# Performance work log

Measured on AMD Instinct MI355X. Metric: run time of the kernel, lower is better.

Reference implementation:

```python
import jax, jax.numpy as jnp
import numpy as np

B, T, C, H = 4, 4096, 2048, 128  # batch, seq, emb_dim, head_size


def setup_inputs() -> dict:
    key = jax.random.key(0)
    k1, k2, k3, k4 = jax.random.split(key, 4)
    idx = jax.random.normal(k1, (B, T, C), dtype=jnp.float32)
    # nn.Linear weight layout: [out_features, in_features]; scale like torch init
    s = 1.0 / np.sqrt(C)
    Wq = jax.random.uniform(k2, (H, C), jnp.float32, -s, s)
    Wk = jax.random.uniform(k3, (H, C), jnp.float32, -s, s)
    Wv = jax.random.uniform(k4, (H, C), jnp.float32, -s, s)
    return {"idx": idx, "Wq": Wq, "Wk": Wk, "Wv": Wv}


def reference(idx, Wq, Wk, Wv):
    b, t, c = idx.shape
    q = jnp.einsum('btc,hc->bth', idx, Wq)  # [B,T,H]
    k = jnp.einsum('btc,hc->bth', idx, Wk)
    v = jnp.einsum('btc,hc->bth', idx, Wv)
    # NOTE: original computes keys @ queries^T and scales by emb_dim**-0.5
    scale = jnp.asarray(c, idx.dtype) ** -0.5
    wei = jnp.einsum('bih,bjh->bij', k, q) * scale  # [B,T,T]
    causal = jnp.tril(jnp.ones((t, t), dtype=bool))
    wei = jnp.where(causal, wei, -jnp.inf)
    wei = jax.nn.softmax(wei, axis=-1)
    return jnp.einsum('bij,bjh->bih', wei, v)  # [B,T,H]
```

## Files before the change

### kernel.cpp

```cpp
#include <hip/hip_runtime.h>
#include <hip/hip_bf16.h>
#include <cstdint>

#define TSEQ 4096
#define CDIM 2048
#define HDIM 128

typedef short bf8v __attribute__((ext_vector_type(8)));
typedef float f4v  __attribute__((ext_vector_type(4)));

__device__ __forceinline__ unsigned short f2b(float f) {
  union { float f; unsigned u; } v; v.f = f;
  unsigned u = v.u;
  return (unsigned short)((u + 0x7fffu + ((u >> 16) & 1u)) >> 16);
}

__device__ __forceinline__ f4v mfma16(bf8v a, bf8v b, f4v c) {
  return __builtin_amdgcn_mfma_f32_16x16x32_bf16(a, b, c, 0, 0, 0);
}

__global__ void wcat_kernel(const float* __restrict__ Wq, const float* __restrict__ Wk,
                            const float* __restrict__ Wv, unsigned short* __restrict__ Wcat) {
  int e = (blockIdx.x * 256 + threadIdx.x) * 4;
  int n = e >> 11;
  int k = e & 2047;
  const float* src;
  if (n < 128)      src = Wq + (size_t)n * CDIM + k;
  else if (n < 256) src = Wk + (size_t)(n - 128) * CDIM + k;
  else              src = Wv + (size_t)(n - 256) * CDIM + k;
  float4 f = *(const float4*)src;
  ushort4 o;
  o.x = f2b(f.x); o.y = f2b(f.y); o.z = f2b(f.z); o.w = f2b(f.w);
  *(ushort4*)(Wcat + e) = o;
}

__global__ __launch_bounds__(512, 6) void proj_gemm(const float* __restrict__ A,
                                                    const unsigned short* __restrict__ Bw,
                                                    unsigned short* __restrict__ QB,
                                                    unsigned short* __restrict__ KA,
                                                    unsigned short* __restrict__ VB) {
  __shared__ union {
    struct { unsigned short As[2][64][40]; unsigned short Bs[2][128][40]; } st;
    unsigned short Ct[64][132];
  } sm;
  const int m0 = blockIdx.x * 64;
  const int y  = blockIdx.y;
  const int n0 = y * 128;
  const int tid = threadIdx.x;
  const int lane = tid & 63;
  const int w = tid >> 6;
  const int wm = (w & 1) * 32, wn = (w >> 1) * 32;
  const int llo = lane & 15, lhi = lane >> 4;

  f4v acc[2][2];
#pragma unroll
  for (int i = 0; i < 2; ++i)
#pragma unroll
    for (int j = 0; j < 2; ++j) acc[i][j] = (f4v){0.f, 0.f, 0.f, 0.f};

  const int arow = tid >> 3, acol = (tid & 7) * 4;
  const int brow = tid >> 2, bcol = (tid & 3) * 8;
  const float* aptr = A + (size_t)(m0 + arow) * CDIM + acol;
  const unsigned short* bptr = Bw + (size_t)(n0 + brow) * CDIM + bcol;

  float4 fa = *(const float4*)(aptr);
  uint4  ub = *(const uint4*)(bptr);
  {
    ushort4 o;
    o.x = f2b(fa.x); o.y = f2b(fa.y); o.z = f2b(fa.z); o.w = f2b(fa.w);
    *(ushort4*)&sm.st.As[0][arow][acol] = o;
    *(uint4*)&sm.st.Bs[0][brow][bcol]   = ub;
  }

  for (int it = 0; it < 64; ++it) {
    const int cur = it & 1;
    __syncthreads();
    if (it < 63) {
      fa = *(const float4*)(aptr + (it + 1) * 32);
      ub = *(const uint4*)(bptr + (it + 1) * 32);
    }
    bf8v af[2], bfr[2];
    af[0]  = *(const bf8v*)&sm.st.As[cur][wm + llo][lhi * 8];
    af[1]  = *(const bf8v*)&sm.st.As[cur][wm + 16 + llo][lhi * 8];
    bfr[0] = *(const bf8v*)&sm.st.Bs[cur][wn + llo][lhi * 8];
    bfr[1] = *(const bf8v*)&sm.st.Bs[cur][wn + 16 + llo][lhi * 8];
#pragma unroll
    for (int i = 0; i < 2; ++i)
#pragma unroll
      for (int j = 0; j < 2; ++j) acc[i][j] = mfma16(af[i], bfr[j], acc[i][j]);
    if (it < 63) {
      ushort4 o;
      o.x = f2b(fa.x); o.y = f2b(fa.y); o.z = f2b(fa.z); o.w = f2b(fa.w);
      int nxt = cur ^ 1;
      *(ushort4*)&sm.st.As[nxt][arow][acol] = o;
      *(uint4*)&sm.st.Bs[nxt][brow][bcol]   = ub;
    }
  }
  __syncthreads();
#pragma unroll
  for (int i = 0; i < 2; ++i)
#pragma unroll
    for (int j = 0; j < 2; ++j)
#pragma unroll
      for (int r = 0; r < 4; ++r)
        sm.Ct[wm + i * 16 + lhi * 4 + r][wn + j * 16 + llo] = f2b(acc[i][j][r]);
  __syncthreads();
  if (y < 2) {
    unsigned short* dst = (y == 0) ? QB : KA;
    const size_t base16 = (size_t)(m0 >> 4);
#pragma unroll
    for (int p = 0; p < 2; ++p) {
      int g = p * 512 + tid;
      int t16l = g >> 8, kk = (g >> 6) & 3, ln = g & 63;
      int lo = ln & 15, hi = ln >> 4;
      bf8v v = *(const bf8v*)&sm.Ct[t16l * 16 + lo][kk * 32 + hi * 8];
      *(bf8v*)(dst + (((base16 + t16l) * 4 + kk) * 64 + ln) * 8) = v;
    }
  } else {
    const size_t base32 = (size_t)(m0 >> 5);
#pragma unroll
    for (int p = 0; p < 3; ++p) {
      int g = p * 512 + tid;
      if (g < 1152) {
        int jbl = g / 576;
        int ht  = (g % 576) >> 6;
        int ln  = g & 63;
        int lo = ln & 15, hi = ln >> 4;
        bf8v v;
        if (ht == 8) {
#pragma unroll
          for (int e = 0; e < 8; ++e) v[e] = (lo == 0) ? (short)0x3F80 : (short)0;
        } else {
#pragma unroll
          for (int e = 0; e < 8; ++e) v[e] = (short)sm.Ct[jbl * 32 + hi * 8 + e][ht * 16 + lo];
        }
        *(bf8v*)(VB + (((base32 + jbl) * 9 + ht) * 512 + (size_t)ln * 8)) = v;
      }
    }
  }
}

__global__ __launch_bounds__(256, 4) void attn6(const unsigned short* __restrict__ QB,
                                                const unsigned short* __restrict__ KA,
                                                const unsigned short* __restrict__ VB,
                                                float* __restrict__ out) {
  __shared__ union SM {
    unsigned short Ps[4][2][16][68];
    struct { float Om[4][16][68]; float Lm[4][16]; } mg;
  } sm;
  const int x = blockIdx.x;
  const int b = x & 3;
  const int u = x >> 2;
  const int g = u >> 6, r0 = u & 63;
  const int s = (g & 1) ? (g * 64 + 63 - r0) : (g * 64 + r0);
  const int lastjt = s >> 2;
  const int tid = threadIdx.x;
  const int w = tid >> 6, lane = tid & 63;
  const int llo = lane & 15, lhi = lane >> 4;
  const float scale = 0.022097086912079608f;

  bf8v aK[4];
  {
    const unsigned short* kp = KA + (size_t)(b * 256 + s) * 2048;
#pragma unroll
    for (int kk = 0; kk < 4; ++kk) aK[kk] = *(const bf8v*)(kp + (kk * 64 + lane) * 8);
  }

  f4v Oacc[9];
#pragma unroll
  for (int nt = 0; nt < 9; ++nt) Oacc[nt] = (f4v){0.f, 0.f, 0.f, 0.f};

  auto computeS = [&](int jtS, int buf) {
    const unsigned short* qp = QB + (size_t)(b * 256 + jtS * 4) * 2048;
#pragma unroll
    for (int ct = 0; ct < 4; ++ct) {
      f4v acc = (f4v){0.f, 0.f, 0.f, 0.f};
#pragma unroll
      for (int kk = 0; kk < 4; ++kk) {
        bf8v bq = *(const bf8v*)(qp + ((ct * 4 + kk) * 64 + lane) * 8);
        acc = mfma16(aK[kk], bq, acc);
      }
#pragma unroll
      for (int r = 0; r < 4; ++r) {
        float sv = acc[r];
        if (jtS == lastjt) {
          int j = jtS * 64 + ct * 16 + llo;
          int i = s * 16 + lhi * 4 + r;
          if (j > i) sv = -3.0e38f;
        }
        sm.Ps[w][buf][lhi * 4 + r][ct * 16 + llo] = f2b(__expf(sv * scale));
      }
    }
  };

  if (w <= lastjt) computeS(w, 0);
  int buf = 0;
  for (int jt = w; jt <= lastjt; jt += 4) {
    bf8v aP0 = *(const bf8v*)&sm.Ps[w][buf][llo][lhi * 8];
    bf8v aP1 = *(const bf8v*)&sm.Ps[w][buf][llo][32 + lhi * 8];
    if (jt + 4 <= lastjt) computeS(jt + 4, buf ^ 1);
    const unsigned short* vp = VB + (size_t)(b * 128 + jt * 2) * 4608;
#pragma unroll
    for (int nt = 0; nt < 9; ++nt) {
      f4v o = Oacc[nt];
      o = mfma16(aP0, *(const bf8v*)(vp + nt * 512 + (size_t)lane * 8), o);
      o = mfma16(aP1, *(const bf8v*)(vp + 4608 + nt * 512 + (size_t)lane * 8), o);
      Oacc[nt] = o;
    }
    buf ^= 1;
  }

#pragma unroll
  for (int half = 0; half < 2; ++half) {
    __syncthreads();
#pragma unroll
    for (int nt = 0; nt < 4; ++nt)
#pragma unroll
      for (int r = 0; r < 4; ++r)
        sm.mg.Om[w][lhi * 4 + r][nt * 16 + llo] = Oacc[half * 4 + nt][r];
    if (half == 0 && llo == 0) {
#pragma unroll
      for (int r = 0; r < 4; ++r) sm.mg.Lm[w][lhi * 4 + r] = Oacc[8][r];
    }
    __syncthreads();
    {
      int row = tid >> 4, c0 = (tid & 15) * 4;
      float L = sm.mg.Lm[0][row] + sm.mg.Lm[1][row] + sm.mg.Lm[2][row] + sm.mg.Lm[3][row];
      float inv = 1.0f / L;
      float* op = out + (size_t)(b * TSEQ + s * 16 + row) * HDIM + half * 64 + c0;
#pragma unroll
      for (int e = 0; e < 4; ++e) {
        float o = sm.mg.Om[0][row][c0 + e] + sm.mg.Om[1][row][c0 + e] +
                  sm.mg.Om[2][row][c0 + e] + sm.mg.Om[3][row][c0 + e];
        op[e] = o * inv;
      }
    }
  }
}

extern "C" void kernel_launch(void* const* d_in, const int* in_sizes, int n_in,
                              void* d_out, int out_size, void* d_ws, size_t ws_size,
                              hipStream_t stream) {
  const float* idx = (const float*)d_in[0];
  const float* Wq  = (const float*)d_in[1];
  const float* Wk  = (const float*)d_in[2];
  const float* Wv  = (const float*)d_in[3];
  float* out = (float*)d_out;
  char* ws = (char*)d_ws;
  unsigned short* Wcat = (unsigned short*)ws;
  unsigned short* QB   = (unsigned short*)(ws + ((size_t)2  << 20));
  unsigned short* KA   = (unsigned short*)(ws + ((size_t)7  << 20));
  unsigned short* VB   = (unsigned short*)(ws + ((size_t)12 << 20));

  wcat_kernel<<<768, 256, 0, stream>>>(Wq, Wk, Wv, Wcat);
  proj_gemm<<<dim3(256, 3), 512, 0, stream>>>(idx, Wcat, QB, KA, VB);
  attn6<<<1024, 256, 0, stream>>>(QB, KA, VB, out);
}
```

Before: 291.1 us.

## Fuse QKV projection into one 64x384 tile with async LDS weight loads

The projection GEMM now computes all three Q/K/V outputs in a single block covering 64 rows by 384 columns, instead of launching three column blocks per row tile. This means the fp32 activation tile is read and converted to bf16 once rather than three times. Weight tiles are loaded straight from global memory into LDS with global_load_lds, using an XOR swizzle to avoid bank conflicts, and the K step grows to 64. The cost is fewer blocks (256), much larger LDS use, and lower occupancy (launch bounds 2 instead of 6).

```diff
diff --git a/kernel.cpp b/kernel.cpp
--- a/kernel.cpp
+++ b/kernel.cpp
@@ -17,6 +17,12 @@
 
 __device__ __forceinline__ f4v mfma16(bf8v a, bf8v b, f4v c) {
   return __builtin_amdgcn_mfma_f32_16x16x32_bf16(a, b, c, 0, 0, 0);
+}
+
+__device__ __forceinline__ void gload_lds16(const void* g, void* l) {
+  __builtin_amdgcn_global_load_lds(
+      (const __attribute__((address_space(1))) unsigned int*)g,
+      (__attribute__((address_space(3))) unsigned int*)l, 16, 0, 0);
 }
 
 __global__ void wcat_kernel(const float* __restrict__ Wq, const float* __restrict__ Wk,
@@ -34,89 +40,114 @@
   *(ushort4*)(Wcat + e) = o;
 }
 
-__global__ __launch_bounds__(512, 6) void proj_gemm(const float* __restrict__ A,
+__global__ __launch_bounds__(512, 2) void proj_gemm(const float* __restrict__ A,
                                                     const unsigned short* __restrict__ Bw,
                                                     unsigned short* __restrict__ QB,
                                                     unsigned short* __restrict__ KA,
                                                     unsigned short* __restrict__ VB) {
   __shared__ union {
-    struct { unsigned short As[2][64][40]; unsigned short Bs[2][128][40]; } st;
-    unsigned short Ct[64][132];
+    struct { unsigned short As[2][64][72]; unsigned short Bs[2][384][64]; } st;
+    unsigned short Ct[64][392];
   } sm;
   const int m0 = blockIdx.x * 64;
-  const int y  = blockIdx.y;
-  const int n0 = y * 128;
   const int tid = threadIdx.x;
   const int lane = tid & 63;
   const int w = tid >> 6;
-  const int wm = (w & 1) * 32, wn = (w >> 1) * 32;
   const int llo = lane & 15, lhi = lane >> 4;
 
-  f4v acc[2][2];
-#pragma unroll
-  for (int i = 0; i < 2; ++i)
-#pragma unroll
-    for (int j = 0; j < 2; ++j) acc[i][j] = (f4v){0.f, 0.f, 0.f, 0.f};
-
-  const int arow = tid >> 3, acol = (tid & 7) * 4;
-  const int brow = tid >> 2, bcol = (tid & 3) * 8;
-  const float* aptr = A + (size_t)(m0 + arow) * CDIM + acol;
-  const unsigned short* bptr = Bw + (size_t)(n0 + brow) * CDIM + bcol;
-
-  float4 fa = *(const float4*)(aptr);
-  uint4  ub = *(const uint4*)(bptr);
-  {
-    ushort4 o;
-    o.x = f2b(fa.x); o.y = f2b(fa.y); o.z = f2b(fa.z); o.w = f2b(fa.w);
-    *(ushort4*)&sm.st.As[0][arow][acol] = o;
-    *(uint4*)&sm.st.Bs[0][brow][bcol]   = ub;
-  }
-
-  for (int it = 0; it < 64; ++it) {
+  f4v acc[4][3];
+#pragma unroll
+  for (int i = 0; i < 4; ++i)
+#pragma unroll
+    for (int j = 0; j < 3; ++j) acc[i][j] = (f4v){0.f, 0.f, 0.f, 0.f};
+
+  const int ar0 = tid >> 4;
+  const int ac0 = (tid & 15) * 4;
+  const float* aptr0 = A + (size_t)(m0 + ar0) * CDIM + ac0;
+  const float* aptr1 = A + (size_t)(m0 + 32 + ar0) * CDIM + ac0;
+
+  const int brow = lane >> 3;
+  const int bgs  = (lane & 7) ^ brow;
+  const unsigned short* bptr = Bw + (size_t)(w * 48 + brow) * CDIM + bgs * 8;
+
+  float4 fa0 = *(const float4*)(aptr0);
+  float4 fa1 = *(const float4*)(aptr1);
+#pragma unroll
+  for (int j = 0; j < 6; ++j)
+    gload_lds16(bptr + (size_t)j * 8 * CDIM, &sm.st.Bs[0][w * 48 + j * 8][0]);
+  {
+    ushort4 o0, o1;
+    o0.x = f2b(fa0.x); o0.y = f2b(fa0.y); o0.z = f2b(fa0.z); o0.w = f2b(fa0.w);
+    o1.x = f2b(fa1.x); o1.y = f2b(fa1.y); o1.z = f2b(fa1.z); o1.w = f2b(fa1.w);
+    *(ushort4*)&sm.st.As[0][ar0][ac0]      = o0;
+    *(ushort4*)&sm.st.As[0][32 + ar0][ac0] = o1;
+  }
+
+  for (int it = 0; it < 32; ++it) {
     const int cur = it & 1;
     __syncthreads();
-    if (it < 63) {
-      fa = *(const float4*)(aptr + (it + 1) * 32);
-      ub = *(const uint4*)(bptr + (it + 1) * 32);
-    }
-    bf8v af[2], bfr[2];
-    af[0]  = *(const bf8v*)&sm.st.As[cur][wm + llo][lhi * 8];
-    af[1]  = *(const bf8v*)&sm.st.As[cur][wm + 16 + llo][lhi * 8];
-    bfr[0] = *(const bf8v*)&sm.st.Bs[cur][wn + llo][lhi * 8];
-    bfr[1] = *(const bf8v*)&sm.st.Bs[cur][wn + 16 + llo][lhi * 8];
-#pragma unroll
-    for (int i = 0; i < 2; ++i)
-#pragma unroll
-      for (int j = 0; j < 2; ++j) acc[i][j] = mfma16(af[i], bfr[j], acc[i][j]);
-    if (it < 63) {
-      ushort4 o;
-      o.x = f2b(fa.x); o.y = f2b(fa.y); o.z = f2b(fa.z); o.w = f2b(fa.w);
-      int nxt = cur ^ 1;
-      *(ushort4*)&sm.st.As[nxt][arow][acol] = o;
-      *(uint4*)&sm.st.Bs[nxt][brow][bcol]   = ub;
-    }
-  }
+    if (it < 31) {
+      fa0 = *(const float4*)(aptr0 + (it + 1) * 64);
+      fa1 = *(const float4*)(aptr1 + (it + 1) * 64);
+      const int nxt = cur ^ 1;
+#pragma unroll
+      for (int j = 0; j < 6; ++j)
+        gload_lds16(bptr + (size_t)j * 8 * CDIM + (it + 1) * 64,
+                    &sm.st.Bs[nxt][w * 48 + j * 8][0]);
+    }
+#pragma unroll
+    for (int kk = 0; kk < 2; ++kk) {
+      bf8v af[4], bf[3];
+#pragma unroll
+      for (int i = 0; i < 4; ++i)
+        af[i] = *(const bf8v*)&sm.st.As[cur][i * 16 + llo][kk * 32 + lhi * 8];
+#pragma unroll
+      for (int j = 0; j < 3; ++j) {
+        const int n = w * 48 + j * 16 + llo;
+        bf[j] = *(const bf8v*)&sm.st.Bs[cur][n][(((kk << 2) + lhi) ^ (llo & 7)) * 8];
+      }
+#pragma unroll
+      for (int i = 0; i < 4; ++i)
+#pragma unroll
+        for (int j = 0; j < 3; ++j) acc[i][j] = mfma16(af[i], bf[j], acc[i][j]);
+    }
+    if (it < 31) {
+      const int nxt = cur ^ 1;
+      ushort4 o0, o1;
+      o0.x = f2b(fa0.x); o0.y = f2b(fa0.y); o0.z = f2b(fa0.z); o0.w = f2b(fa0.w);
+      o1.x = f2b(fa1.x); o1.y = f2b(fa1.y); o1.z = f2b(fa1.z); o1.w = f2b(fa1.w);
+      *(ushort4*)&sm.st.As[nxt][ar0][ac0]      = o0;
+      *(ushort4*)&sm.st.As[nxt][32 + ar0][ac0] = o1;
+    }
+  }
+
   __syncthreads();
 #pragma unroll
-  for (int i = 0; i < 2; ++i)
-#pragma unroll
-    for (int j = 0; j < 2; ++j)
+  for (int i = 0; i < 4; ++i)
+#pragma unroll
+    for (int j = 0; j < 3; ++j)
 #pragma unroll
       for (int r = 0; r < 4; ++r)
-        sm.Ct[wm + i * 16 + lhi * 4 + r][wn + j * 16 + llo] = f2b(acc[i][j][r]);
+        sm.Ct[i * 16 + lhi * 4 + r][w * 48 + j * 16 + llo] = f2b(acc[i][j][r]);
   __syncthreads();
-  if (y < 2) {
-    unsigned short* dst = (y == 0) ? QB : KA;
+
+  {
     const size_t base16 = (size_t)(m0 >> 4);
 #pragma unroll
-    for (int p = 0; p < 2; ++p) {
-      int g = p * 512 + tid;
-      int t16l = g >> 8, kk = (g >> 6) & 3, ln = g & 63;
-      int lo = ln & 15, hi = ln >> 4;
-      bf8v v = *(const bf8v*)&sm.Ct[t16l * 16 + lo][kk * 32 + hi * 8];
-      *(bf8v*)(dst + (((base16 + t16l) * 4 + kk) * 64 + ln) * 8) = v;
-    }
-  } else {
+    for (int yy = 0; yy < 2; ++yy) {
+      unsigned short* dst = yy ? KA : QB;
+      const int colb = yy * 128;
+#pragma unroll
+      for (int p = 0; p < 2; ++p) {
+        int g = p * 512 + tid;
+        int t16l = g >> 8, kk2 = (g >> 6) & 3, ln = g & 63;
+        int lo = ln & 15, hi = ln >> 4;
+        bf8v v = *(const bf8v*)&sm.Ct[t16l * 16 + lo][colb + kk2 * 32 + hi * 8];
+        *(bf8v*)(dst + (((base16 + t16l) * 4 + kk2) * 64 + ln) * 8) = v;
+      }
+    }
+  }
+  {
     const size_t base32 = (size_t)(m0 >> 5);
 #pragma unroll
     for (int p = 0; p < 3; ++p) {
@@ -132,7 +163,7 @@
           for (int e = 0; e < 8; ++e) v[e] = (lo == 0) ? (short)0x3F80 : (short)0;
         } else {
 #pragma unroll
-          for (int e = 0; e < 8; ++e) v[e] = (short)sm.Ct[jbl * 32 + hi * 8 + e][ht * 16 + lo];
+          for (int e = 0; e < 8; ++e) v[e] = (short)sm.Ct[jbl * 32 + hi * 8 + e][256 + ht * 16 + lo];
         }
         *(bf8v*)(VB + (((base32 + jbl) * 9 + ht) * 512 + (size_t)ln * 8)) = v;
       }
@@ -253,6 +284,6 @@
   unsigned short* VB   = (unsigned short*)(ws + ((size_t)12 << 20));
 
   wcat_kernel<<<768, 256, 0, stream>>>(Wq, Wk, Wv, Wcat);
-  proj_gemm<<<dim3(256, 3), 512, 0, stream>>>(idx, Wcat, QB, KA, VB);
+  proj_gemm<<<256, 512, 0, stream>>>(idx, Wcat, QB, KA, VB);
   attn6<<<1024, 256, 0, stream>>>(QB, KA, VB, out);
 }
```

After: 282.8 us. 2.8% less time.

## Fuse QKV projection into one pass per row tile with MFMA-packed weights

Applied to the files above, without the earlier changes.

The weight-conversion kernel now writes the concatenated bf16 weights pre-swizzled into MFMA fragment order. The projection GEMM drops the 3-way grid split and LDS staging: each 64-row block computes all 384 output columns, and each wave loads its fp32 activation fragments straight from global memory into registers. This reads the large activation tensor once instead of three times and removes per-iteration barriers. In exchange it uses more accumulator registers, has lower occupancy, and does uncoalesced global reads of the B fragments, relying on L2 hits.

```diff
diff --git a/kernel.cpp b/kernel.cpp
--- a/kernel.cpp
+++ b/kernel.cpp
@@ -21,102 +21,106 @@
 
 __global__ void wcat_kernel(const float* __restrict__ Wq, const float* __restrict__ Wk,
                             const float* __restrict__ Wv, unsigned short* __restrict__ Wcat) {
-  int e = (blockIdx.x * 256 + threadIdx.x) * 4;
-  int n = e >> 11;
-  int k = e & 2047;
+  int c = blockIdx.x * 256 + threadIdx.x;
+  int lane = c & 63;
+  int kkg  = (c >> 6) & 63;
+  int nb   = c >> 12;
+  int n  = nb * 16 + (lane & 15);
+  int k0 = kkg * 32 + (lane >> 4) * 8;
   const float* src;
-  if (n < 128)      src = Wq + (size_t)n * CDIM + k;
-  else if (n < 256) src = Wk + (size_t)(n - 128) * CDIM + k;
-  else              src = Wv + (size_t)(n - 256) * CDIM + k;
-  float4 f = *(const float4*)src;
-  ushort4 o;
-  o.x = f2b(f.x); o.y = f2b(f.y); o.z = f2b(f.z); o.w = f2b(f.w);
-  *(ushort4*)(Wcat + e) = o;
-}
-
-__global__ __launch_bounds__(512, 6) void proj_gemm(const float* __restrict__ A,
+  if (n < 128)      src = Wq + (size_t)n * CDIM + k0;
+  else if (n < 256) src = Wk + (size_t)(n - 128) * CDIM + k0;
+  else              src = Wv + (size_t)(n - 256) * CDIM + k0;
+  float4 f0 = ((const float4*)src)[0];
+  float4 f1 = ((const float4*)src)[1];
+  bf8v o;
+  o[0] = (short)f2b(f0.x); o[1] = (short)f2b(f0.y);
+  o[2] = (short)f2b(f0.z); o[3] = (short)f2b(f0.w);
+  o[4] = (short)f2b(f1.x); o[5] = (short)f2b(f1.y);
+  o[6] = (short)f2b(f1.z); o[7] = (short)f2b(f1.w);
+  *(bf8v*)(Wcat + (size_t)c * 8) = o;
+}
+
+__global__ __launch_bounds__(512, 2) void proj_gemm(const float* __restrict__ A,
                                                     const unsigned short* __restrict__ Bw,
                                                     unsigned short* __restrict__ QB,
                                                     unsigned short* __restrict__ KA,
                                                     unsigned short* __restrict__ VB) {
-  __shared__ union {
-    struct { unsigned short As[2][64][40]; unsigned short Bs[2][128][40]; } st;
-    unsigned short Ct[64][132];
-  } sm;
+  __shared__ unsigned short Ct[64][392];
   const int m0 = blockIdx.x * 64;
-  const int y  = blockIdx.y;
-  const int n0 = y * 128;
   const int tid = threadIdx.x;
   const int lane = tid & 63;
   const int w = tid >> 6;
-  const int wm = (w & 1) * 32, wn = (w >> 1) * 32;
+  const int sub = w & 3;
+  const int cg  = w >> 2;
   const int llo = lane & 15, lhi = lane >> 4;
 
-  f4v acc[2][2];
-#pragma unroll
-  for (int i = 0; i < 2; ++i)
-#pragma unroll
-    for (int j = 0; j < 2; ++j) acc[i][j] = (f4v){0.f, 0.f, 0.f, 0.f};
-
-  const int arow = tid >> 3, acol = (tid & 7) * 4;
-  const int brow = tid >> 2, bcol = (tid & 3) * 8;
-  const float* aptr = A + (size_t)(m0 + arow) * CDIM + acol;
-  const unsigned short* bptr = Bw + (size_t)(n0 + brow) * CDIM + bcol;
-
-  float4 fa = *(const float4*)(aptr);
-  uint4  ub = *(const uint4*)(bptr);
+  f4v acc[12];
+#pragma unroll
+  for (int j = 0; j < 12; ++j) acc[j] = (f4v){0.f, 0.f, 0.f, 0.f};
+
+  const float* ap = A + (size_t)(m0 + sub * 16 + llo) * CDIM + lhi * 8;
+
+  float4 fa00 = *(const float4*)(ap);
+  float4 fa01 = *(const float4*)(ap + 4);
+  float4 fa10 = *(const float4*)(ap + 32);
+  float4 fa11 = *(const float4*)(ap + 36);
+
+  const unsigned short* bbase = Bw + (size_t)(cg * 12) * 64 * 64 * 8 + (size_t)lane * 8;
+
+  for (int it = 0; it < 32; ++it) {
+    bf8v af[2];
+    af[0][0] = (short)f2b(fa00.x); af[0][1] = (short)f2b(fa00.y);
+    af[0][2] = (short)f2b(fa00.z); af[0][3] = (short)f2b(fa00.w);
+    af[0][4] = (short)f2b(fa01.x); af[0][5] = (short)f2b(fa01.y);
+    af[0][6] = (short)f2b(fa01.z); af[0][7] = (short)f2b(fa01.w);
+    af[1][0] = (short)f2b(fa10.x); af[1][1] = (short)f2b(fa10.y);
+    af[1][2] = (short)f2b(fa10.z); af[1][3] = (short)f2b(fa10.w);
+    af[1][4] = (short)f2b(fa11.x); af[1][5] = (short)f2b(fa11.y);
+    af[1][6] = (short)f2b(fa11.z); af[1][7] = (short)f2b(fa11.w);
+    if (it < 31) {
+      const float* apn = ap + (it + 1) * 64;
+      fa00 = *(const float4*)(apn);
+      fa01 = *(const float4*)(apn + 4);
+      fa10 = *(const float4*)(apn + 32);
+      fa11 = *(const float4*)(apn + 36);
+    }
+#pragma unroll
+    for (int kk = 0; kk < 2; ++kk) {
+      const int kkg = it * 2 + kk;
+      bf8v bf[12];
+#pragma unroll
+      for (int j = 0; j < 12; ++j)
+        bf[j] = *(const bf8v*)(bbase + ((size_t)j * 64 + kkg) * 64 * 8);
+#pragma unroll
+      for (int j = 0; j < 12; ++j) acc[j] = mfma16(af[kk], bf[j], acc[j]);
+    }
+  }
+
+#pragma unroll
+  for (int j = 0; j < 12; ++j)
+#pragma unroll
+    for (int r = 0; r < 4; ++r)
+      Ct[sub * 16 + lhi * 4 + r][cg * 192 + j * 16 + llo] = f2b(acc[j][r]);
+  __syncthreads();
+
   {
-    ushort4 o;
-    o.x = f2b(fa.x); o.y = f2b(fa.y); o.z = f2b(fa.z); o.w = f2b(fa.w);
-    *(ushort4*)&sm.st.As[0][arow][acol] = o;
-    *(uint4*)&sm.st.Bs[0][brow][bcol]   = ub;
-  }
-
-  for (int it = 0; it < 64; ++it) {
-    const int cur = it & 1;
-    __syncthreads();
-    if (it < 63) {
-      fa = *(const float4*)(aptr + (it + 1) * 32);
-      ub = *(const uint4*)(bptr + (it + 1) * 32);
-    }
-    bf8v af[2], bfr[2];
-    af[0]  = *(const bf8v*)&sm.st.As[cur][wm + llo][lhi * 8];
-    af[1]  = *(const bf8v*)&sm.st.As[cur][wm + 16 + llo][lhi * 8];
-    bfr[0] = *(const bf8v*)&sm.st.Bs[cur][wn + llo][lhi * 8];
-    bfr[1] = *(const bf8v*)&sm.st.Bs[cur][wn + 16 + llo][lhi * 8];
-#pragma unroll
-    for (int i = 0; i < 2; ++i)
-#pragma unroll
-      for (int j = 0; j < 2; ++j) acc[i][j] = mfma16(af[i], bfr[j], acc[i][j]);
-    if (it < 63) {
-      ushort4 o;
-      o.x = f2b(fa.x); o.y = f2b(fa.y); o.z = f2b(fa.z); o.w = f2b(fa.w);
-      int nxt = cur ^ 1;
-      *(ushort4*)&sm.st.As[nxt][arow][acol] = o;
-      *(uint4*)&sm.st.Bs[nxt][brow][bcol]   = ub;
-    }
-  }
-  __syncthreads();
-#pragma unroll
-  for (int i = 0; i < 2; ++i)
-#pragma unroll
-    for (int j = 0; j < 2; ++j)
-#pragma unroll
-      for (int r = 0; r < 4; ++r)
-        sm.Ct[wm + i * 16 + lhi * 4 + r][wn + j * 16 + llo] = f2b(acc[i][j][r]);
-  __syncthreads();
-  if (y < 2) {
-    unsigned short* dst = (y == 0) ? QB : KA;
     const size_t base16 = (size_t)(m0 >> 4);
 #pragma unroll
-    for (int p = 0; p < 2; ++p) {
-      int g = p * 512 + tid;
-      int t16l = g >> 8, kk = (g >> 6) & 3, ln = g & 63;
-      int lo = ln & 15, hi = ln >> 4;
-      bf8v v = *(const bf8v*)&sm.Ct[t16l * 16 + lo][kk * 32 + hi * 8];
-      *(bf8v*)(dst + (((base16 + t16l) * 4 + kk) * 64 + ln) * 8) = v;
-    }
-  } else {
+    for (int yy = 0; yy < 2; ++yy) {
+      unsigned short* dst = yy ? KA : QB;
+      const int colb = yy * 128;
+#pragma unroll
+      for (int p = 0; p < 2; ++p) {
+        int g = p * 512 + tid;
+        int t16l = g >> 8, kk2 = (g >> 6) & 3, ln = g & 63;
+        int lo = ln & 15, hi = ln >> 4;
+        bf8v v = *(const bf8v*)&Ct[t16l * 16 + lo][colb + kk2 * 32 + hi * 8];
+        *(bf8v*)(dst + (((base16 + t16l) * 4 + kk2) * 64 + ln) * 8) = v;
+      }
+    }
+  }
+  {
     const size_t base32 = (size_t)(m0 >> 5);
 #pragma unroll
     for (int p = 0; p < 3; ++p) {
@@ -132,7 +136,7 @@
           for (int e = 0; e < 8; ++e) v[e] = (lo == 0) ? (short)0x3F80 : (short)0;
         } else {
 #pragma unroll
-          for (int e = 0; e < 8; ++e) v[e] = (short)sm.Ct[jbl * 32 + hi * 8 + e][ht * 16 + lo];
+          for (int e = 0; e < 8; ++e) v[e] = (short)Ct[jbl * 32 + hi * 8 + e][256 + ht * 16 + lo];
         }
         *(bf8v*)(VB + (((base32 + jbl) * 9 + ht) * 512 + (size_t)ln * 8)) = v;
       }
@@ -252,7 +256,7 @@
   unsigned short* KA   = (unsigned short*)(ws + ((size_t)7  << 20));
   unsigned short* VB   = (unsigned short*)(ws + ((size_t)12 << 20));
 
-  wcat_kernel<<<768, 256, 0, stream>>>(Wq, Wk, Wv, Wcat);
-  proj_gemm<<<dim3(256, 3), 512, 0, stream>>>(idx, Wcat, QB, KA, VB);
+  wcat_kernel<<<384, 256, 0, stream>>>(Wq, Wk, Wv, Wcat);
+  proj_gemm<<<256, 512, 0, stream>>>(idx, Wcat, QB, KA, VB);
   attn6<<<1024, 256, 0, stream>>>(QB, KA, VB, out);
 }
```

Measured after the change: 337.2 us. 15.9% more time.

## Load projection weights directly into LDS with swizzle and double K-tile depth

Applied to the files above, without the earlier changes.

The projection GEMM now uses global_load_lds to stream the bf16 weight tile straight into shared memory, bypassing registers. It uses an XOR swizzle on the B tile so the MFMA fragment reads avoid bank conflicts. The K tile per iteration doubles from 32 to 64, which halves the number of barriers and loop iterations. Shared memory use grows, which could lower occupancy under the 6-block launch bound.

```diff
diff --git a/kernel.cpp b/kernel.cpp
--- a/kernel.cpp
+++ b/kernel.cpp
@@ -17,6 +17,12 @@
 
 __device__ __forceinline__ f4v mfma16(bf8v a, bf8v b, f4v c) {
   return __builtin_amdgcn_mfma_f32_16x16x32_bf16(a, b, c, 0, 0, 0);
+}
+
+__device__ __forceinline__ void gload_lds16(const void* g, void* l) {
+  __builtin_amdgcn_global_load_lds(
+      (const __attribute__((address_space(1))) unsigned int*)g,
+      (__attribute__((address_space(3))) unsigned int*)l, 16, 0, 0);
 }
 
 __global__ void wcat_kernel(const float* __restrict__ Wq, const float* __restrict__ Wk,
@@ -40,12 +46,12 @@
                                                     unsigned short* __restrict__ KA,
                                                     unsigned short* __restrict__ VB) {
   __shared__ union {
-    struct { unsigned short As[2][64][40]; unsigned short Bs[2][128][40]; } st;
+    struct { unsigned short As[2][64][72]; unsigned short Bs[2][128][64]; } st;
     unsigned short Ct[64][132];
   } sm;
   const int m0 = blockIdx.x * 64;
   const int y  = blockIdx.y;
-  const int n0 = y * 128;
+  const int n0g = y * 128;
   const int tid = threadIdx.x;
   const int lane = tid & 63;
   const int w = tid >> 6;
@@ -58,42 +64,57 @@
 #pragma unroll
     for (int j = 0; j < 2; ++j) acc[i][j] = (f4v){0.f, 0.f, 0.f, 0.f};
 
-  const int arow = tid >> 3, acol = (tid & 7) * 4;
-  const int brow = tid >> 2, bcol = (tid & 3) * 8;
-  const float* aptr = A + (size_t)(m0 + arow) * CDIM + acol;
-  const unsigned short* bptr = Bw + (size_t)(n0 + brow) * CDIM + bcol;
-
-  float4 fa = *(const float4*)(aptr);
-  uint4  ub = *(const uint4*)(bptr);
+  const int ar0 = tid >> 4;
+  const int ac0 = (tid & 15) * 4;
+  const float* aptr0 = A + (size_t)(m0 + ar0) * CDIM + ac0;
+  const float* aptr1 = A + (size_t)(m0 + 32 + ar0) * CDIM + ac0;
+
+  const int brow = lane >> 3;
+  const int bgs  = (lane & 7) ^ brow;
+  const unsigned short* bptr = Bw + (size_t)(n0g + w * 16 + brow) * CDIM + bgs * 8;
+
+  float4 fa0 = *(const float4*)(aptr0);
+  float4 fa1 = *(const float4*)(aptr1);
+  gload_lds16(bptr,            &sm.st.Bs[0][w * 16][0]);
+  gload_lds16(bptr + 8 * CDIM, &sm.st.Bs[0][w * 16 + 8][0]);
   {
-    ushort4 o;
-    o.x = f2b(fa.x); o.y = f2b(fa.y); o.z = f2b(fa.z); o.w = f2b(fa.w);
-    *(ushort4*)&sm.st.As[0][arow][acol] = o;
-    *(uint4*)&sm.st.Bs[0][brow][bcol]   = ub;
-  }
-
-  for (int it = 0; it < 64; ++it) {
+    ushort4 o0, o1;
+    o0.x = f2b(fa0.x); o0.y = f2b(fa0.y); o0.z = f2b(fa0.z); o0.w = f2b(fa0.w);
+    o1.x = f2b(fa1.x); o1.y = f2b(fa1.y); o1.z = f2b(fa1.z); o1.w = f2b(fa1.w);
+    *(ushort4*)&sm.st.As[0][ar0][ac0]      = o0;
+    *(ushort4*)&sm.st.As[0][32 + ar0][ac0] = o1;
+  }
+
+  for (int it = 0; it < 32; ++it) {
     const int cur = it & 1;
     __syncthreads();
-    if (it < 63) {
-      fa = *(const float4*)(aptr + (it + 1) * 32);
-      ub = *(const uint4*)(bptr + (it + 1) * 32);
-    }
-    bf8v af[2], bfr[2];
-    af[0]  = *(const bf8v*)&sm.st.As[cur][wm + llo][lhi * 8];
-    af[1]  = *(const bf8v*)&sm.st.As[cur][wm + 16 + llo][lhi * 8];
-    bfr[0] = *(const bf8v*)&sm.st.Bs[cur][wn + llo][lhi * 8];
-    bfr[1] = *(const bf8v*)&sm.st.Bs[cur][wn + 16 + llo][lhi * 8];
-#pragma unroll
-    for (int i = 0; i < 2; ++i)
-#pragma unroll
-      for (int j = 0; j < 2; ++j) acc[i][j] = mfma16(af[i], bfr[j], acc[i][j]);
-    if (it < 63) {
-      ushort4 o;
-      o.x = f2b(fa.x); o.y = f2b(fa.y); o.z = f2b(fa.z); o.w = f2b(fa.w);
-      int nxt = cur ^ 1;
-      *(ushort4*)&sm.st.As[nxt][arow][acol] = o;
-      *(uint4*)&sm.st.Bs[nxt][brow][bcol]   = ub;
+    if (it < 31) {
+      fa0 = *(const float4*)(aptr0 + (it + 1) * 64);
+      fa1 = *(const float4*)(aptr1 + (it + 1) * 64);
+      const int nxt = cur ^ 1;
+      gload_lds16(bptr + (it + 1) * 64,            &sm.st.Bs[nxt][w * 16][0]);
+      gload_lds16(bptr + 8 * CDIM + (it + 1) * 64, &sm.st.Bs[nxt][w * 16 + 8][0]);
+    }
+#pragma unroll
+    for (int kk = 0; kk < 2; ++kk) {
+      bf8v af[2], bfr[2];
+      af[0] = *(const bf8v*)&sm.st.As[cur][wm + llo][kk * 32 + lhi * 8];
+      af[1] = *(const bf8v*)&sm.st.As[cur][wm + 16 + llo][kk * 32 + lhi * 8];
+      const int bofs = (((kk << 2) + lhi) ^ (llo & 7)) * 8;
+      bfr[0] = *(const bf8v*)&sm.st.Bs[cur][wn + llo][bofs];
+      bfr[1] = *(const bf8v*)&sm.st.Bs[cur][wn + 16 + llo][bofs];
+#pragma unroll
+      for (int i = 0; i < 2; ++i)
+#pragma unroll
+        for (int j = 0; j < 2; ++j) acc[i][j] = mfma16(af[i], bfr[j], acc[i][j]);
+    }
+    if (it < 31) {
+      const int nxt = cur ^ 1;
+      ushort4 o0, o1;
+      o0.x = f2b(fa0.x); o0.y = f2b(fa0.y); o0.z = f2b(fa0.z); o0.w = f2b(fa0.w);
+      o1.x = f2b(fa1.x); o1.y = f2b(fa1.y); o1.z = f2b(fa1.z); o1.w = f2b(fa1.w);
+      *(ushort4*)&sm.st.As[nxt][ar0][ac0]      = o0;
+      *(ushort4*)&sm.st.As[nxt][32 + ar0][ac0] = o1;
     }
   }
   __syncthreads();
```

Result: no change. 286.2 us (-1.7%).
